# Performance work log

Hardware: AMD Instinct MI355X
Metric: run time of the kernel (lower is better)

Reference implementation:

```python
import jax, jax.numpy as jnp
import numpy as np

N_NODES = 20000


def _gcn_norm(edge_index, n):
    """Add self loops and compute symmetric normalization (PyG GCNConv default)."""
    loop = jnp.arange(n, dtype=edge_index.dtype)
    src = jnp.concatenate([edge_index[0], loop])  # [E+N]
    dst = jnp.concatenate([edge_index[1], loop])  # [E+N]
    deg = jax.ops.segment_sum(jnp.ones_like(dst, dtype=jnp.float32), dst, num_segments=n)
    inv_sqrt = deg ** -0.5  # deg >= 1 thanks to self loops
    norm = inv_sqrt[src] * inv_sqrt[dst]  # [E+N]
    return src, dst, norm


def _gcn_conv(x, W, b, src, dst, norm, n):
    xw = x @ W                                   # [N, out] dense transform
    msg = xw[src] * norm[:, None]                # gather + scale  [E+N, out]
    out = jax.ops.segment_sum(msg, dst, num_segments=n)  # scatter-add
    return out + b


def setup_inputs() -> dict:
    key = jax.random.key(0)
    ks = jax.random.split(key, 6)
    n, f = N_NODES, 256
    x = jax.random.normal(ks[0], (n, f), dtype=jnp.float32)
    edge_index = jax.random.randint(ks[1], (2, 320000), 0, n, dtype=jnp.int64)
    def lin(k, fi, fo):
        return jax.random.normal(k, (fi, fo), dtype=jnp.float32) * (1.0 / np.sqrt(fi))
    return {
        "x": x,
        "edge_index": edge_index,
        "W1": lin(ks[2], 256, 1024), "b1": jnp.zeros((1024,), jnp.float32),
        "W2": lin(ks[3], 1024, 512), "b2": jnp.zeros((512,), jnp.float32),
        "W3": lin(ks[4], 512, 128), "b3": jnp.zeros((128,), jnp.float32),
        "Wc": lin(ks[5], 128, 64), "bc": jnp.zeros((64,), jnp.float32),
    }


def reference(x, edge_index, W1, b1, W2, b2, W3, b3, Wc, bc):
    n = x.shape[0]
    src, dst, norm = _gcn_norm(edge_index, n)  # same graph for all layers
    h = jax.nn.relu(_gcn_conv(x, W1, b1, src, dst, norm, n))
    h = jax.nn.relu(_gcn_conv(h, W2, b2, src, dst, norm, n))
    h = jax.nn.relu(_gcn_conv(h, W3, b3, src, dst, norm, n))
    return h @ Wc + bc  # classifier logits [N, num_classes]
```

## Files before the change

kernel.cpp:

```cpp
#include <hip/hip_runtime.h>
#include <hip/hip_fp16.h>

typedef _Float16 half8 __attribute__((ext_vector_type(8)));
typedef _Float16 half4 __attribute__((ext_vector_type(4)));
typedef float floatx4 __attribute__((ext_vector_type(4)));


__device__ __forceinline__ void gload_lds16(const _Float16* g, _Float16* l) {
    __builtin_amdgcn_global_load_lds(
        (__attribute__((address_space(1))) void*)(g),
        (__attribute__((address_space(3))) void*)(l), 16, 0, 0);
}

__global__ void hist_kernel(const int* __restrict__ dst, int* __restrict__ cnt, int E) {
    int e = blockIdx.x * blockDim.x + threadIdx.x;
    if (e < E) atomicAdd(&cnt[dst[e]], 1);
}

__global__ void bsum_isd_kernel(const int* __restrict__ cnt, int* __restrict__ bsum,
                                float* __restrict__ isd, int n) {
    int i = blockIdx.x * 256 + threadIdx.x;
    int v = 0;
    if (i < n) {
        v = cnt[i];
        isd[i] = rsqrtf((float)(v + 1));
    }
#pragma unroll
    for (int o = 32; o > 0; o >>= 1) v += __shfl_down(v, o);
    __shared__ int ws[4];
    int lane = threadIdx.x & 63, w = threadIdx.x >> 6;
    if (lane == 0) ws[w] = v;
    __syncthreads();
    if (threadIdx.x == 0) bsum[blockIdx.x] = ws[0] + ws[1] + ws[2] + ws[3];
}

__global__ void bscan_kernel(int* __restrict__ bsum, int nb) {
    __shared__ int sh[256];
    int t = threadIdx.x;
    int v = (t < nb) ? bsum[t] : 0;
    sh[t] = v;
    __syncthreads();
    for (int o = 1; o < 256; o <<= 1) {
        int u = (t >= o) ? sh[t - o] : 0;
        __syncthreads();
        sh[t] += u;
        __syncthreads();
    }
    if (t < nb) bsum[t] = sh[t] - v;
}

__global__ void rowptr_kernel(const int* __restrict__ cnt, const int* __restrict__ bsum,
                              int* __restrict__ row_ptr, int n, int E) {
    __shared__ int sh[256];
    int t = threadIdx.x;
    int i = blockIdx.x * 256 + t;
    int v = (i < n) ? cnt[i] : 0;
    sh[t] = v;
    __syncthreads();
    for (int o = 1; o < 256; o <<= 1) {
        int u = (t >= o) ? sh[t - o] : 0;
        __syncthreads();
        sh[t] += u;
        __syncthreads();
    }
    if (i < n) row_ptr[i] = bsum[blockIdx.x] + sh[t] - v;
    if (blockIdx.x == 0 && t == 0) row_ptr[n] = E;
}

__global__ void place_kernel(const int* __restrict__ src, const int* __restrict__ dst,
                             const float* __restrict__ isd, const int* __restrict__ row_ptr,
                             int* __restrict__ pos, int* __restrict__ s_src,
                             float* __restrict__ s_nrm, int E) {
    int e = blockIdx.x * blockDim.x + threadIdx.x;
    if (e < E) {
        int s = src[e], d = dst[e];
        int p = row_ptr[d] + atomicAdd(&pos[d], 1);
        s_src[p] = s;
        s_nrm[p] = isd[s] * isd[d];
    }
}

__global__ void convert_all_kernel(const float* __restrict__ W1, const float* __restrict__ W2,
                                   const float* __restrict__ W3, const float* __restrict__ Wc,
                                   _Float16* __restrict__ w1t, _Float16* __restrict__ w2t,
                                   _Float16* __restrict__ w3t, _Float16* __restrict__ wct,
                                   const float4* __restrict__ x, half4* __restrict__ xh,
                                   int n4) {
    int idx = blockIdx.x * 256 + threadIdx.x;
    if (idx < 262144) {
        int o = idx >> 8, i2 = idx & 255;
        w1t[idx] = (_Float16)W1[(size_t)i2 * 1024 + o];
        return;
    }
    idx -= 262144;
    if (idx < 524288) {
        int o = idx >> 10, i2 = idx & 1023;
        w2t[idx] = (_Float16)W2[(size_t)i2 * 512 + o];
        return;
    }
    idx -= 524288;
    if (idx < 65536) {
        int o = idx >> 9, i2 = idx & 511;
        w3t[idx] = (_Float16)W3[(size_t)i2 * 128 + o];
        return;
    }
    idx -= 65536;
    if (idx < 8192) {
        int o = idx >> 7, i2 = idx & 127;
        wct[idx] = (_Float16)Wc[(size_t)i2 * 64 + o];
        return;
    }
    idx -= 8192;
    if (idx < n4) {
        float4 v = x[idx];
        half4 o = { (_Float16)v.x, (_Float16)v.y, (_Float16)v.z, (_Float16)v.w };
        xh[idx] = o;
    }
}

template <int LPN, bool BIASRELU>
__global__ __launch_bounds__(256)
void aggv_kernel(const half8* __restrict__ xin, half8* __restrict__ xout,
                 const int* __restrict__ row_ptr, const int* __restrict__ s_src,
                 const float* __restrict__ s_nrm, const float* __restrict__ isd,
                 const float* __restrict__ bias, int n) {
    int t = blockIdx.x * blockDim.x + threadIdx.x;
    int i = t / LPN;
    int r = t % LPN;
    if (i >= n) return;
    float w = isd[i]; w *= w;
    half8 v = xin[(size_t)i * LPN + r];
    float a0[8], a1[8], a2[8], a3[8];
#pragma unroll
    for (int j = 0; j < 8; ++j) {
        a0[j] = (float)v[j] * w;
        a1[j] = 0.f; a2[j] = 0.f; a3[j] = 0.f;
    }
    int c = row_ptr[i], end = row_ptr[i + 1];
    for (; c + 8 <= end; c += 8) {
        int s0 = s_src[c],     s1 = s_src[c + 1], s2 = s_src[c + 2], s3 = s_src[c + 3];
        int s4 = s_src[c + 4], s5 = s_src[c + 5], s6 = s_src[c + 6], s7 = s_src[c + 7];
        float n0 = s_nrm[c],     n1 = s_nrm[c + 1], n2 = s_nrm[c + 2], n3 = s_nrm[c + 3];
        float n4 = s_nrm[c + 4], n5 = s_nrm[c + 5], n6 = s_nrm[c + 6], n7 = s_nrm[c + 7];
        half8 v0 = xin[(size_t)s0 * LPN + r];
        half8 v1 = xin[(size_t)s1 * LPN + r];
        half8 v2 = xin[(size_t)s2 * LPN + r];
        half8 v3 = xin[(size_t)s3 * LPN + r];
        half8 v4 = xin[(size_t)s4 * LPN + r];
        half8 v5 = xin[(size_t)s5 * LPN + r];
        half8 v6 = xin[(size_t)s6 * LPN + r];
        half8 v7 = xin[(size_t)s7 * LPN + r];
#pragma unroll
        for (int j = 0; j < 8; ++j) {
            a0[j] = fmaf((float)v0[j], n0, a0[j]);
            a1[j] = fmaf((float)v1[j], n1, a1[j]);
            a2[j] = fmaf((float)v2[j], n2, a2[j]);
            a3[j] = fmaf((float)v3[j], n3, a3[j]);
            a0[j] = fmaf((float)v4[j], n4, a0[j]);
            a1[j] = fmaf((float)v5[j], n5, a1[j]);
            a2[j] = fmaf((float)v6[j], n6, a2[j]);
            a3[j] = fmaf((float)v7[j], n7, a3[j]);
        }
    }
    for (; c + 2 <= end; c += 2) {
        int s0 = s_src[c], s1 = s_src[c + 1];
        float n0 = s_nrm[c], n1 = s_nrm[c + 1];
        half8 v0 = xin[(size_t)s0 * LPN + r];
        half8 v1 = xin[(size_t)s1 * LPN + r];
#pragma unroll
        for (int j = 0; j < 8; ++j) {
            a0[j] = fmaf((float)v0[j], n0, a0[j]);
            a1[j] = fmaf((float)v1[j], n1, a1[j]);
        }
    }
    if (c < end) {
        int s0 = s_src[c];
        float n0 = s_nrm[c];
        half8 v0 = xin[(size_t)s0 * LPN + r];
#pragma unroll
        for (int j = 0; j < 8; ++j) a0[j] = fmaf((float)v0[j], n0, a0[j]);
    }
    half8 o;
#pragma unroll
    for (int j = 0; j < 8; ++j) {
        float s = (a0[j] + a1[j]) + (a2[j] + a3[j]);
        if (BIASRELU) s = fmaxf(s + bias[r * 8 + j], 0.f);
        o[j] = (_Float16)s;
    }
    xout[(size_t)i * LPN + r] = o;
}

template <int ES, bool BIASRELU>
__global__ __launch_bounds__(256)
void aggw_kernel(const half8* __restrict__ xin, half8* __restrict__ xout,
                 const int* __restrict__ row_ptr, const int* __restrict__ s_src,
                 const float* __restrict__ s_nrm, const float* __restrict__ isd,
                 const float* __restrict__ bias, int n) {
    const int C8 = 64 / ES;
    int i = blockIdx.x * 4 + (threadIdx.x >> 6);
    if (i >= n) return;
    int lane = threadIdx.x & 63;
    int c8 = lane % C8;
    int es = lane / C8;
    float a0[8], a1[8];
    if (es == 0) {
        float w = isd[i]; w *= w;
        half8 v = xin[(size_t)i * C8 + c8];
#pragma unroll
        for (int j = 0; j < 8; ++j) { a0[j] = (float)v[j] * w; a1[j] = 0.f; }
    } else {
#pragma unroll
        for (int j = 0; j < 8; ++j) { a0[j] = 0.f; a1[j] = 0.f; }
    }
    int end = row_ptr[i + 1];
    int c = row_ptr[i] + es;
    for (; c + 3 * ES < end; c += 4 * ES) {
        int s0 = s_src[c];
        int s1 = s_src[c + ES];
        int s2 = s_src[c + 2 * ES];
        int s3 = s_src[c + 3 * ES];
        float n0 = s_nrm[c];
        float n1 = s_nrm[c + ES];
        float n2 = s_nrm[c + 2 * ES];
        float n3 = s_nrm[c + 3 * ES];
        half8 v0 = xin[(size_t)s0 * C8 + c8];
        half8 v1 = xin[(size_t)s1 * C8 + c8];
        half8 v2 = xin[(size_t)s2 * C8 + c8];
        half8 v3 = xin[(size_t)s3 * C8 + c8];
#pragma unroll
        for (int j = 0; j < 8; ++j) {
            a0[j] = fmaf((float)v0[j], n0, a0[j]);
            a1[j] = fmaf((float)v1[j], n1, a1[j]);
            a0[j] = fmaf((float)v2[j], n2, a0[j]);
            a1[j] = fmaf((float)v3[j], n3, a1[j]);
        }
    }
    for (; c < end; c += ES) {
        int s0 = s_src[c];
        float n0 = s_nrm[c];
        half8 v0 = xin[(size_t)s0 * C8 + c8];
#pragma unroll
        for (int j = 0; j < 8; ++j) a0[j] = fmaf((float)v0[j], n0, a0[j]);
    }
#pragma unroll
    for (int j = 0; j < 8; ++j) a0[j] += a1[j];
#pragma unroll
    for (int m = C8; m < 64; m <<= 1)
#pragma unroll
        for (int j = 0; j < 8; ++j) a0[j] += __shfl_xor(a0[j], m);
    if (es == 0) {
        half8 o;
#pragma unroll
        for (int j = 0; j < 8; ++j) {
            float s = a0[j];
            if (BIASRELU) s = fmaxf(s + bias[c8 * 8 + j], 0.f);
            o[j] = (_Float16)s;
        }
        xout[(size_t)i * C8 + c8] = o;
    }
}

template <bool BIAS, bool RELU, bool OUT_HALF>
__global__ __launch_bounds__(256, 6)
void hgemm_kernel(const _Float16* __restrict__ A, const _Float16* __restrict__ Bt,
                  const float* __restrict__ bias, void* __restrict__ C,
                  int M, int K, int Ncout, int ldc, int gy) {
    __shared__ _Float16 As[128 * 64];
    __shared__ _Float16 Bs[64 * 64];

    int nwg = gridDim.x;
    int orig = blockIdx.x;
    int q = nwg >> 3, r = nwg & 7;
    int xcd = orig & 7, seq = orig >> 3;
    int wgid = (xcd < r ? xcd * (q + 1) : r * (q + 1) + (xcd - r) * q) + seq;
    int bx = wgid / gy, by = wgid % gy;

    const int tid = threadIdx.x;
    const int wave = tid >> 6, lane = tid & 63;
    const int l15 = lane & 15, lk = lane >> 4;
    const int wr = wave >> 1, wc = wave & 1;
    const int bm = bx * 128, bn = by * 64;

    const int sk_swz = (((tid & 7) ^ ((tid >> 3) & 7)) << 3);
    const _Float16* aSrc = A + (size_t)(bm + (tid >> 3)) * K + sk_swz;
    const _Float16* bSrc = Bt + (size_t)(bn + (tid >> 3)) * K + sk_swz;

    const int rowA = wr * 64 + l15;
    const int rowB = wc * 32 + l15;
    const int xorK = (l15 & 7) << 3;

    floatx4 acc[4][2] = {};

    const int nt = K >> 6;
    for (int t = 0; t < nt; ++t) {
        int k0 = t << 6;
#pragma unroll
        for (int i = 0; i < 4; ++i)
            gload_lds16(aSrc + k0 + (size_t)i * 32 * K, As + (i * 256 + tid) * 8);
#pragma unroll
        for (int i = 0; i < 2; ++i)
            gload_lds16(bSrc + k0 + (size_t)i * 32 * K, Bs + (i * 256 + tid) * 8);
        __syncthreads();
#pragma unroll
        for (int ks = 0; ks < 2; ++ks) {
            const int kidx = ((lk << 3) + (ks << 5)) ^ xorK;
            half8 af[4], bf[2];
#pragma unroll
            for (int mi = 0; mi < 4; ++mi)
                af[mi] = *(const half8*)(&As[(rowA + mi * 16) * 64 + kidx]);
#pragma unroll
            for (int ni = 0; ni < 2; ++ni)
                bf[ni] = *(const half8*)(&Bs[(rowB + ni * 16) * 64 + kidx]);
#pragma unroll
            for (int mi = 0; mi < 4; ++mi)
#pragma unroll
                for (int ni = 0; ni < 2; ++ni)
                    acc[mi][ni] = __builtin_amdgcn_mfma_f32_16x16x32_f16(
                        af[mi], bf[ni], acc[mi][ni], 0, 0, 0);
        }
        __syncthreads();
    }

#pragma unroll
    for (int mi = 0; mi < 4; ++mi) {
#pragma unroll
        for (int ni = 0; ni < 2; ++ni) {
            int col = bn + wc * 32 + ni * 16 + l15;
            int row0 = bm + wr * 64 + mi * 16 + lk * 4;
            floatx4 vv = acc[mi][ni];
            if (BIAS) {
                float bb = (col < Ncout) ? bias[col] : 0.f;
                vv[0] += bb; vv[1] += bb; vv[2] += bb; vv[3] += bb;
            }
            if (RELU) {
                vv[0] = fmaxf(vv[0], 0.f); vv[1] = fmaxf(vv[1], 0.f);
                vv[2] = fmaxf(vv[2], 0.f); vv[3] = fmaxf(vv[3], 0.f);
            }
            if (col < Ncout) {
#pragma unroll
                for (int rr = 0; rr < 4; ++rr) {
                    int row = row0 + rr;
                    if (row < M) {
                        if (OUT_HALF)
                            ((__half*)C)[(size_t)row * ldc + col] = __float2half(vv[rr]);
                        else
                            ((float*)C)[(size_t)row * ldc + col] = vv[rr];
                    }
                }
            }
        }
    }
}

extern "C" void kernel_launch(void* const* d_in, const int* in_sizes, int n_in,
                              void* d_out, int out_size, void* d_ws, size_t ws_size,
                              hipStream_t stream) {
    const float* x  = (const float*)d_in[0];
    const int*   ei = (const int*)d_in[1];
    const float* W1 = (const float*)d_in[2];
    const float* b1 = (const float*)d_in[3];
    const float* W2 = (const float*)d_in[4];
    const float* b2 = (const float*)d_in[5];
    const float* W3 = (const float*)d_in[6];
    const float* b3 = (const float*)d_in[7];
    const float* Wc = (const float*)d_in[8];
    const float* bc = (const float*)d_in[9];
    float* out = (float*)d_out;

    const int n = in_sizes[0] / 256;
    const int E = in_sizes[1] / 2;
    const int* src = ei;
    const int* dst = ei + E;
    const int Mpad = ((n + 127) / 128) * 128;
    const int gx = Mpad / 128;
    const int nb = (n + 255) / 256;

    size_t off = 0;
    auto take = [&](size_t bytes) -> void* {
        void* p = (char*)d_ws + off;
        off += (bytes + 255) & ~(size_t)255;
        return p;
    };
    float* isd     = (float*)take((size_t)n * 4);
    int*   cnt     = (int*)take((size_t)n * 4);
    int*   pos     = (int*)take((size_t)n * 4);
    int*   row_ptr = (int*)take((size_t)(n + 1) * 4);
    int*   bsum    = (int*)take((size_t)256 * 4);
    int*   s_src   = (int*)take((size_t)E * 4);
    float* s_nrm   = (float*)take((size_t)E * 4);
    _Float16* xh   = (_Float16*)take((size_t)n * 256 * 2);
    _Float16* a1h  = (_Float16*)take((size_t)Mpad * 256 * 2);
    _Float16* h1h  = (_Float16*)take((size_t)Mpad * 1024 * 2);
    _Float16* g2h  = (_Float16*)take((size_t)Mpad * 512 * 2);
    _Float16* a2h  = (_Float16*)take((size_t)Mpad * 512 * 2);
    _Float16* g3h  = (_Float16*)take((size_t)Mpad * 128 * 2);
    _Float16* a3h  = (_Float16*)take((size_t)Mpad * 128 * 2);
    _Float16* w1t  = (_Float16*)take((size_t)1024 * 256 * 2);
    _Float16* w2t  = (_Float16*)take((size_t)512 * 1024 * 2);
    _Float16* w3t  = (_Float16*)take((size_t)128 * 512 * 2);
    _Float16* wct  = (_Float16*)take((size_t)64 * 128 * 2);

    hipMemsetAsync(cnt, 0, (size_t)n * 4, stream);
    hipMemsetAsync(pos, 0, (size_t)n * 4, stream);
    hist_kernel<<<(E + 255) / 256, 256, 0, stream>>>(dst, cnt, E);
    bsum_isd_kernel<<<nb, 256, 0, stream>>>(cnt, bsum, isd, n);
    bscan_kernel<<<1, 256, 0, stream>>>(bsum, nb);
    rowptr_kernel<<<nb, 256, 0, stream>>>(cnt, bsum, row_ptr, n, E);
    place_kernel<<<(E + 255) / 256, 256, 0, stream>>>(src, dst, isd, row_ptr, pos,
                                                      s_src, s_nrm, E);

    int n4 = n * 256 / 4;
    int conv_total = 860160 + n4;
    convert_all_kernel<<<(conv_total + 255) / 256, 256, 0, stream>>>(
        W1, W2, W3, Wc, w1t, w2t, w3t, wct, (const float4*)x, (half4*)xh, n4);

    aggw_kernel<2, false><<<(n + 3) / 4, 256, 0, stream>>>(
        (const half8*)xh, (half8*)a1h, row_ptr, s_src, s_nrm, isd, nullptr, n);
    hgemm_kernel<true, true, true><<<gx * 16, 256, 0, stream>>>(
        a1h, w1t, b1, h1h, n, 256, 1024, 1024, 16);

    hgemm_kernel<false, false, true><<<gx * 8, 256, 0, stream>>>(
        h1h, w2t, nullptr, g2h, n, 1024, 512, 512, 8);
    aggv_kernel<64, true><<<(n * 64 + 255) / 256, 256, 0, stream>>>(
        (const half8*)g2h, (half8*)a2h, row_ptr, s_src, s_nrm, isd, b2, n);

    hgemm_kernel<false, false, true><<<gx * 2, 256, 0, stream>>>(
        a2h, w3t, nullptr, g3h, n, 512, 128, 128, 2);
    aggw_kernel<4, true><<<(n + 3) / 4, 256, 0, stream>>>(
        (const half8*)g3h, (half8*)a3h, row_ptr, s_src, s_nrm, isd, b3, n);

    hgemm_kernel<true, false, false><<<gx * 1, 256, 0, stream>>>(
        a3h, wct, bc, out, n, 128, 64, 64, 1);
}
```

Measured before the change: 216.7 us.

## Fuse last aggregation with classifier and use 128x128 tiles for layer-1 GEMM

The layer-3 neighbour aggregation, bias and ReLU now feed straight into the 128->64 classifier inside one kernel, using lane shuffles and scalar FMAs against the fp16 weights. This removes the a3h intermediate buffer and one GEMM launch. The first-layer GEMM switches to a new 128x128-tile variant with a larger shared-memory B tile to improve operand reuse. In exchange it runs at lower occupancy and launches half as many blocks.

Result: slower. 247.7 us (+14.3%).

```diff
diff --git a/kernel.cpp b/kernel.cpp
--- a/kernel.cpp
+++ b/kernel.cpp
@@ -260,6 +260,83 @@
     }
 }
 
+__global__ __launch_bounds__(256)
+void aggclf_kernel(const half8* __restrict__ xin, float* __restrict__ outp,
+                   const int* __restrict__ row_ptr, const int* __restrict__ s_src,
+                   const float* __restrict__ s_nrm, const float* __restrict__ isd,
+                   const float* __restrict__ b3, const _Float16* __restrict__ wct,
+                   const float* __restrict__ bc, int n) {
+    const int ES = 4, C8 = 16;
+    int i = blockIdx.x * 4 + (threadIdx.x >> 6);
+    if (i >= n) return;
+    int lane = threadIdx.x & 63;
+    int c8 = lane & 15;
+    int es = lane >> 4;
+    float a0[8], a1[8];
+    if (es == 0) {
+        float w = isd[i]; w *= w;
+        half8 v = xin[(size_t)i * C8 + c8];
+#pragma unroll
+        for (int j = 0; j < 8; ++j) { a0[j] = (float)v[j] * w; a1[j] = 0.f; }
+    } else {
+#pragma unroll
+        for (int j = 0; j < 8; ++j) { a0[j] = 0.f; a1[j] = 0.f; }
+    }
+    int end = row_ptr[i + 1];
+    int c = row_ptr[i] + es;
+    for (; c + 3 * ES < end; c += 4 * ES) {
+        int s0 = s_src[c];
+        int s1 = s_src[c + ES];
+        int s2 = s_src[c + 2 * ES];
+        int s3 = s_src[c + 3 * ES];
+        float n0 = s_nrm[c];
+        float n1 = s_nrm[c + ES];
+        float n2 = s_nrm[c + 2 * ES];
+        float n3 = s_nrm[c + 3 * ES];
+        half8 v0 = xin[(size_t)s0 * C8 + c8];
+        half8 v1 = xin[(size_t)s1 * C8 + c8];
+        half8 v2 = xin[(size_t)s2 * C8 + c8];
+        half8 v3 = xin[(size_t)s3 * C8 + c8];
+#pragma unroll
+        for (int j = 0; j < 8; ++j) {
+            a0[j] = fmaf((float)v0[j], n0, a0[j]);
+            a1[j] = fmaf((float)v1[j], n1, a1[j]);
+            a0[j] = fmaf((float)v2[j], n2, a0[j]);
+            a1[j] = fmaf((float)v3[j], n3, a1[j]);
+        }
+    }
+    for (; c < end; c += ES) {
+        int s0 = s_src[c];
+        float n0 = s_nrm[c];
+        half8 v0 = xin[(size_t)s0 * C8 + c8];
+#pragma unroll
+        for (int j = 0; j < 8; ++j) a0[j] = fmaf((float)v0[j], n0, a0[j]);
+    }
+#pragma unroll
+    for (int j = 0; j < 8; ++j) a0[j] += a1[j];
+#pragma unroll
+    for (int m = 16; m < 64; m <<= 1)
+#pragma unroll
+        for (int j = 0; j < 8; ++j) a0[j] += __shfl_xor(a0[j], m);
+
+    float r[8];
+#pragma unroll
+    for (int j = 0; j < 8; ++j) r[j] = fmaxf(a0[j] + b3[c8 * 8 + j], 0.f);
+
+    const half8* wrow = (const half8*)(wct + (size_t)lane * 128);
+    float acc = bc[lane];
+#pragma unroll
+    for (int d8 = 0; d8 < 16; ++d8) {
+        half8 wv = wrow[d8];
+#pragma unroll
+        for (int j = 0; j < 8; ++j) {
+            float rv = __shfl(r[j], d8);
+            acc = fmaf(rv, (float)wv[j], acc);
+        }
+    }
+    outp[(size_t)i * 64 + lane] = acc;
+}
+
 template <bool BIAS, bool RELU, bool OUT_HALF>
 __global__ __launch_bounds__(256, 6)
 void hgemm_kernel(const _Float16* __restrict__ A, const _Float16* __restrict__ Bt,
@@ -326,6 +403,98 @@
 #pragma unroll
         for (int ni = 0; ni < 2; ++ni) {
             int col = bn + wc * 32 + ni * 16 + l15;
+            int row0 = bm + wr * 64 + mi * 16 + lk * 4;
+            floatx4 vv = acc[mi][ni];
+            if (BIAS) {
+                float bb = (col < Ncout) ? bias[col] : 0.f;
+                vv[0] += bb; vv[1] += bb; vv[2] += bb; vv[3] += bb;
+            }
+            if (RELU) {
+                vv[0] = fmaxf(vv[0], 0.f); vv[1] = fmaxf(vv[1], 0.f);
+                vv[2] = fmaxf(vv[2], 0.f); vv[3] = fmaxf(vv[3], 0.f);
+            }
+            if (col < Ncout) {
+#pragma unroll
+                for (int rr = 0; rr < 4; ++rr) {
+                    int row = row0 + rr;
+                    if (row < M) {
+                        if (OUT_HALF)
+                            ((__half*)C)[(size_t)row * ldc + col] = __float2half(vv[rr]);
+                        else
+                            ((float*)C)[(size_t)row * ldc + col] = vv[rr];
+                    }
+                }
+            }
+        }
+    }
+}
+
+template <bool BIAS, bool RELU, bool OUT_HALF>
+__global__ __launch_bounds__(256, 4)
+void hgemm128_kernel(const _Float16* __restrict__ A, const _Float16* __restrict__ Bt,
+                     const float* __restrict__ bias, void* __restrict__ C,
+                     int M, int K, int Ncout, int ldc, int gy) {
+    __shared__ _Float16 As[128 * 64];
+    __shared__ _Float16 Bs[128 * 64];
+
+    int nwg = gridDim.x;
+    int orig = blockIdx.x;
+    int q = nwg >> 3, r = nwg & 7;
+    int xcd = orig & 7, seq = orig >> 3;
+    int wgid = (xcd < r ? xcd * (q + 1) : r * (q + 1) + (xcd - r) * q) + seq;
+    int bx = wgid / gy, by = wgid % gy;
+
+    const int tid = threadIdx.x;
+    const int wave = tid >> 6, lane = tid & 63;
+    const int l15 = lane & 15, lk = lane >> 4;
+    const int wr = wave >> 1, wc = wave & 1;
+    const int bm = bx * 128, bn = by * 128;
+
+    const int sk_swz = (((tid & 7) ^ ((tid >> 3) & 7)) << 3);
+    const _Float16* aSrc = A + (size_t)(bm + (tid >> 3)) * K + sk_swz;
+    const _Float16* bSrc = Bt + (size_t)(bn + (tid >> 3)) * K + sk_swz;
+
+    const int rowA = wr * 64 + l15;
+    const int rowB = wc * 64 + l15;
+    const int xorK = (l15 & 7) << 3;
+
+    floatx4 acc[4][4] = {};
+
+    const int nt = K >> 6;
+    for (int t = 0; t < nt; ++t) {
+        int k0 = t << 6;
+#pragma unroll
+        for (int i = 0; i < 4; ++i)
+            gload_lds16(aSrc + k0 + (size_t)i * 32 * K, As + (i * 256 + tid) * 8);
+#pragma unroll
+        for (int i = 0; i < 4; ++i)
+            gload_lds16(bSrc + k0 + (size_t)i * 32 * K, Bs + (i * 256 + tid) * 8);
+        __syncthreads();
+#pragma unroll
+        for (int ks = 0; ks < 2; ++ks) {
+            const int kidx = ((lk << 3) + (ks << 5)) ^ xorK;
+            half8 af[4], bf[4];
+#pragma unroll
+            for (int mi = 0; mi < 4; ++mi)
+                af[mi] = *(const half8*)(&As[(rowA + mi * 16) * 64 + kidx]);
+#pragma unroll
+            for (int ni = 0; ni < 4; ++ni)
+                bf[ni] = *(const half8*)(&Bs[(rowB + ni * 16) * 64 + kidx]);
+#pragma unroll
+            for (int mi = 0; mi < 4; ++mi)
+#pragma unroll
+                for (int ni = 0; ni < 4; ++ni)
+                    acc[mi][ni] = __builtin_amdgcn_mfma_f32_16x16x32_f16(
+                        af[mi], bf[ni], acc[mi][ni], 0, 0, 0);
+        }
+        __syncthreads();
+    }
+
+#pragma unroll
+    for (int mi = 0; mi < 4; ++mi) {
+#pragma unroll
+        for (int ni = 0; ni < 4; ++ni) {
+            int col = bn + wc * 64 + ni * 16 + l15;
             int row0 = bm + wr * 64 + mi * 16 + lk * 4;
             floatx4 vv = acc[mi][ni];
             if (BIAS) {
@@ -394,7 +563,6 @@
     _Float16* g2h  = (_Float16*)take((size_t)Mpad * 512 * 2);
     _Float16* a2h  = (_Float16*)take((size_t)Mpad * 512 * 2);
     _Float16* g3h  = (_Float16*)take((size_t)Mpad * 128 * 2);
-    _Float16* a3h  = (_Float16*)take((size_t)Mpad * 128 * 2);
     _Float16* w1t  = (_Float16*)take((size_t)1024 * 256 * 2);
     _Float16* w2t  = (_Float16*)take((size_t)512 * 1024 * 2);
     _Float16* w3t  = (_Float16*)take((size_t)128 * 512 * 2);
@@ -416,8 +584,8 @@
 
     aggw_kernel<2, false><<<(n + 3) / 4, 256, 0, stream>>>(
         (const half8*)xh, (half8*)a1h, row_ptr, s_src, s_nrm, isd, nullptr, n);
-    hgemm_kernel<true, true, true><<<gx * 16, 256, 0, stream>>>(
-        a1h, w1t, b1, h1h, n, 256, 1024, 1024, 16);
+    hgemm128_kernel<true, true, true><<<gx * 8, 256, 0, stream>>>(
+        a1h, w1t, b1, h1h, n, 256, 1024, 1024, 8);
 
     hgemm_kernel<false, false, true><<<gx * 8, 256, 0, stream>>>(
         h1h, w2t, nullptr, g2h, n, 1024, 512, 512, 8);
@@ -426,9 +594,6 @@
 
     hgemm_kernel<false, false, true><<<gx * 2, 256, 0, stream>>>(
         a2h, w3t, nullptr, g3h, n, 512, 128, 128, 2);
-    aggw_kernel<4, true><<<(n + 3) / 4, 256, 0, stream>>>(
-        (const half8*)g3h, (half8*)a3h, row_ptr, s_src, s_nrm, isd, b3, n);
-
-    hgemm_kernel<true, false, false><<<gx * 1, 256, 0, stream>>>(
-        a3h, wct, bc, out, n, 128, 64, 64, 1);
-}
+    aggclf_kernel<<<(n + 3) / 4, 256, 0, stream>>>(
+        (const half8*)g3h, out, row_ptr, s_src, s_nrm, isd, b3, wct, bc, n);
+}
```
